# Optimization experiments

Measured on AMD Instinct MI355X. Metric: run time of the kernel, lower is better.

## Reference

```python
import jax, jax.numpy as jnp
import numpy as np

SIGMA = 5.0
KSIZE = 31  # int(6*sigma+1), odd
CHANNEL = 3

def build_gaussian_kernel(size, sigma):
    coords = jnp.arange(size, dtype=jnp.float32) - size // 2
    g = jnp.exp(-coords ** 2 / (2.0 * sigma ** 2))
    g = g / g.sum()
    k2d = g[:, None] * g[None, :]            # (k, k)
    # depthwise kernel: (O=C, I/g=1, k, k)
    return jnp.broadcast_to(k2d[None, None], (CHANNEL, 1, size, size))

def depthwise_blur(x, kernel):
    # x: (B, C, H, W); kernel: (C, 1, k, k); groups = C, SAME-style padding k//2
    pad = KSIZE // 2
    return jax.lax.conv_general_dilated(
        x, kernel,
        window_strides=(1, 1),
        padding=((pad, pad), (pad, pad)),
        dimension_numbers=("NCHW", "OIHW", "NCHW"),
        feature_group_count=CHANNEL,
    )

def setup_inputs() -> dict:
    key = jax.random.key(0)
    k1, k2 = jax.random.split(key)
    B, C, H, W = 16, 3, 512, 512
    background = jax.random.uniform(k1, (B, C, H, W), dtype=jnp.float32)
    insatance = jax.random.uniform(k2, (B, C, H, W), dtype=jnp.float32)
    gaussian_kernel = build_gaussian_kernel(KSIZE, SIGMA)
    return {"background": background, "insatance": insatance,
            "gaussian_kernel": gaussian_kernel}

def reference(background, insatance, gaussian_kernel):
    # retinex_decompose(background): only illumination1 is used downstream
    bg_log = jnp.log1p(background)
    illumination1 = depthwise_blur(bg_log, gaussian_kernel)
    # retinex_decompose(insatance): reflectance2 = log1p(ins) - blur(log1p(ins))
    ins_log = jnp.log1p(insatance)
    illumination2 = depthwise_blur(ins_log, gaussian_kernel)
    reflectance2 = ins_log - illumination2
    # adjust_illumination(reflectance2, illumination1)
    img_log = reflectance2 + illumination1
    img_corrected = jnp.clip(jnp.expm1(img_log), 0.0, 1.0)
    return img_corrected
```

## Files before the change

### kernel.cpp

```cpp
#include <hip/hip_runtime.h>


constexpr int W_    = 512;
constexpr int H_    = 512;
constexpr int NIMG  = 48;
constexpr int NROWS = NIMG * H_;

__device__ constexpr float G[31] = {
    8.8805851e-04f, 1.5861066e-03f, 2.7217699e-03f, 4.4874399e-03f,
    7.1084368e-03f, 1.0818767e-02f, 1.5820117e-02f, 2.2226435e-02f,
    3.0002549e-02f, 3.8911209e-02f, 4.8486352e-02f, 5.8048702e-02f,
    6.6771901e-02f, 7.3794364e-02f, 7.8357552e-02f, 7.9940480e-02f,
    7.8357552e-02f, 7.3794364e-02f, 6.6771901e-02f, 5.8048702e-02f,
    4.8486352e-02f, 3.8911209e-02f, 3.0002549e-02f, 2.2226435e-02f,
    1.5820117e-02f, 1.0818767e-02f, 7.1084368e-03f, 4.4874399e-03f,
    2.7217699e-03f, 1.5861066e-03f, 8.8805851e-04f};

__global__ __launch_bounds__(128) void hblur(const float* bg,
                                             const float* __restrict__ ins,
                                             float* tmp) {
  __shared__ __align__(16) float sh[544];
  const int tid = threadIdx.x;
  const size_t base = (size_t)blockIdx.x * W_;

  float4* s4w = (float4*)sh;
  if (tid < 8) {
    int s = (tid < 4) ? tid : (128 + tid);
    s4w[s] = make_float4(0.f, 0.f, 0.f, 0.f);
  }
  {
    float4 b = ((const float4*)(bg + base))[tid];
    float4 n = ((const float4*)(ins + base))[tid];
    float4 v;
    v.x = __logf(1.f + b.x) - __logf(1.f + n.x);
    v.y = __logf(1.f + b.y) - __logf(1.f + n.y);
    v.z = __logf(1.f + b.z) - __logf(1.f + n.z);
    v.w = __logf(1.f + b.w) - __logf(1.f + n.w);
    s4w[tid + 4] = v;
  }
  __syncthreads();

  float win[36];
  const float4* s4 = (const float4*)sh;
#pragma unroll
  for (int k = 0; k < 9; ++k) {
    float4 v = s4[tid + k];
    win[4 * k + 0] = v.x; win[4 * k + 1] = v.y;
    win[4 * k + 2] = v.z; win[4 * k + 3] = v.w;
  }
  float4 acc = make_float4(0.f, 0.f, 0.f, 0.f);
#pragma unroll
  for (int c = 0; c < 31; ++c) {
    acc.x += G[c] * win[1 + c];
    acc.y += G[c] * win[2 + c];
    acc.z += G[c] * win[3 + c];
    acc.w += G[c] * win[4 + c];
  }
  ((float4*)(tmp + base))[tid] = acc;
}

__global__ __launch_bounds__(256) void vblur(const float* __restrict__ tmp,
                                             const float* __restrict__ ins,
                                             float* __restrict__ out) {
  const int tx = threadIdx.x;
  const int x  = blockIdx.x * 64 + tx;
  const int y0 = blockIdx.y * 32 + threadIdx.y * 8;
  const size_t base = (size_t)blockIdx.z * ((size_t)H_ * W_);

  float acc[8] = {0.f, 0.f, 0.f, 0.f, 0.f, 0.f, 0.f, 0.f};
#pragma unroll
  for (int j = 0; j < 38; ++j) {
    const int yy = y0 - 15 + j;
    const float v = (yy >= 0 && yy < H_) ? tmp[base + (size_t)yy * W_ + x] : 0.f;
#pragma unroll
    for (int p = 0; p < 8; ++p) {
      const int c = j - p;
      if (c >= 0 && c < 31) acc[p] += G[c] * v;
    }
  }
#pragma unroll
  for (int p = 0; p < 8; ++p) {
    const size_t idx = base + (size_t)(y0 + p) * W_ + x;
    const float il = __logf(1.f + ins[idx]);
    float r = __expf(il + acc[p]) - 1.f;
    r = fminf(fmaxf(r, 0.f), 1.f);
    out[idx] = r;
  }
}

extern "C" void kernel_launch(void* const* d_in, const int* in_sizes, int n_in,
                              void* d_out, int out_size, void* d_ws, size_t ws_size,
                              hipStream_t stream) {
  const float* bg  = (const float*)d_in[0];
  const float* ins = (const float*)d_in[1];
  float* out = (float*)d_out;

  const size_t need = (size_t)NROWS * W_ * sizeof(float);
  float* tmp = (ws_size >= need) ? (float*)d_ws : (float*)d_in[0];

  hblur<<<dim3(NROWS), dim3(128), 0, stream>>>(bg, ins, tmp);
  vblur<<<dim3(8, 16, NIMG), dim3(64, 4, 1), 0, stream>>>(tmp, ins, out);
}
```

Measured before the change: 162.0 us.

## Fuse horizontal and vertical blur into one tiled kernel using shared memory

```diff
diff --git a/kernel.cpp b/kernel.cpp
--- a/kernel.cpp
+++ b/kernel.cpp
@@ -1,10 +1,13 @@
 #include <hip/hip_runtime.h>
 
 
-constexpr int W_    = 512;
-constexpr int H_    = 512;
-constexpr int NIMG  = 48;
-constexpr int NROWS = NIMG * H_;
+constexpr int W_ = 512, H_ = 512;
+constexpr int NIMG = 48;
+constexpr int TW = 64, TH = 64;
+constexpr int R_ = TH + 30;
+constexpr int CSLOT = 24;
+constexpr int DSTRIDE = 25;
+constexpr int HSTRIDE = 17;
 
 __device__ constexpr float G[31] = {
     8.8805851e-04f, 1.5861066e-03f, 2.7217699e-03f, 4.4874399e-03f,
@@ -16,75 +19,92 @@
     1.5820117e-02f, 1.0818767e-02f, 7.1084368e-03f, 4.4874399e-03f,
     2.7217699e-03f, 1.5861066e-03f, 8.8805851e-04f};
 
-__global__ __launch_bounds__(128) void hblur(const float* bg,
-                                             const float* __restrict__ ins,
-                                             float* tmp) {
-  __shared__ __align__(16) float sh[544];
+__global__ __launch_bounds__(256) void retinex_fused(const float* __restrict__ bg,
+                                                     const float* __restrict__ ins,
+                                                     float* __restrict__ out) {
+  __shared__ float4 sd[R_ * DSTRIDE];
+  __shared__ float4 sh[R_ * HSTRIDE];
+
   const int tid = threadIdx.x;
-  const size_t base = (size_t)blockIdx.x * W_;
+  const int x0 = blockIdx.x * TW;
+  const int y0 = blockIdx.y * TH;
+  const size_t base = (size_t)blockIdx.z * ((size_t)H_ * W_);
 
-  float4* s4w = (float4*)sh;
-  if (tid < 8) {
-    int s = (tid < 4) ? tid : (128 + tid);
-    s4w[s] = make_float4(0.f, 0.f, 0.f, 0.f);
-  }
-  {
-    float4 b = ((const float4*)(bg + base))[tid];
-    float4 n = ((const float4*)(ins + base))[tid];
-    float4 v;
-    v.x = __logf(1.f + b.x) - __logf(1.f + n.x);
-    v.y = __logf(1.f + b.y) - __logf(1.f + n.y);
-    v.z = __logf(1.f + b.z) - __logf(1.f + n.z);
-    v.w = __logf(1.f + b.w) - __logf(1.f + n.w);
-    s4w[tid + 4] = v;
+#pragma unroll
+  for (int it = 0; it < 9; ++it) {
+    const int idx = tid + 256 * it;
+    if (idx < R_ * CSLOT) {
+      const int r = idx / CSLOT;
+      const int c = idx - r * CSLOT;
+      const int y = y0 - 15 + r;
+      const int gx = x0 - 16 + 4 * c;
+      float4 v = make_float4(0.f, 0.f, 0.f, 0.f);
+      if ((unsigned)y < (unsigned)H_ && (unsigned)gx < (unsigned)W_) {
+        const size_t a = base + (size_t)y * W_ + gx;
+        const float4 b = *(const float4*)(bg + a);
+        const float4 n = *(const float4*)(ins + a);
+        v.x = __logf(1.f + b.x) - __logf(1.f + n.x);
+        v.y = __logf(1.f + b.y) - __logf(1.f + n.y);
+        v.z = __logf(1.f + b.z) - __logf(1.f + n.z);
+        v.w = __logf(1.f + b.w) - __logf(1.f + n.w);
+      }
+      sd[r * DSTRIDE + c] = v;
+    }
   }
   __syncthreads();
 
-  float win[36];
-  const float4* s4 = (const float4*)sh;
 #pragma unroll
-  for (int k = 0; k < 9; ++k) {
-    float4 v = s4[tid + k];
-    win[4 * k + 0] = v.x; win[4 * k + 1] = v.y;
-    win[4 * k + 2] = v.z; win[4 * k + 3] = v.w;
-  }
-  float4 acc = make_float4(0.f, 0.f, 0.f, 0.f);
+  for (int it = 0; it < 3; ++it) {
+    const int idx = tid + 256 * it;
+    if (idx < R_ * 8) {
+      const int r = idx >> 3;
+      const int w = idx & 7;
+      float win[40];
+      const float4* p = &sd[r * DSTRIDE + 2 * w];
 #pragma unroll
-  for (int c = 0; c < 31; ++c) {
-    acc.x += G[c] * win[1 + c];
-    acc.y += G[c] * win[2 + c];
-    acc.z += G[c] * win[3 + c];
-    acc.w += G[c] * win[4 + c];
-  }
-  ((float4*)(tmp + base))[tid] = acc;
-}
-
-__global__ __launch_bounds__(256) void vblur(const float* __restrict__ tmp,
-                                             const float* __restrict__ ins,
-                                             float* __restrict__ out) {
-  const int tx = threadIdx.x;
-  const int x  = blockIdx.x * 64 + tx;
-  const int y0 = blockIdx.y * 32 + threadIdx.y * 8;
-  const size_t base = (size_t)blockIdx.z * ((size_t)H_ * W_);
-
-  float acc[8] = {0.f, 0.f, 0.f, 0.f, 0.f, 0.f, 0.f, 0.f};
+      for (int k = 0; k < 10; ++k) {
+        const float4 v = p[k];
+        win[4 * k + 0] = v.x; win[4 * k + 1] = v.y;
+        win[4 * k + 2] = v.z; win[4 * k + 3] = v.w;
+      }
+      float o[8];
 #pragma unroll
-  for (int j = 0; j < 38; ++j) {
-    const int yy = y0 - 15 + j;
-    const float v = (yy >= 0 && yy < H_) ? tmp[base + (size_t)yy * W_ + x] : 0.f;
+      for (int e = 0; e < 8; ++e) {
+        float a = 0.f;
 #pragma unroll
-    for (int p = 0; p < 8; ++p) {
-      const int c = j - p;
-      if (c >= 0 && c < 31) acc[p] += G[c] * v;
+        for (int c = 0; c < 31; ++c) a += G[c] * win[e + 1 + c];
+        o[e] = a;
+      }
+      sh[r * HSTRIDE + 2 * w]     = make_float4(o[0], o[1], o[2], o[3]);
+      sh[r * HSTRIDE + 2 * w + 1] = make_float4(o[4], o[5], o[6], o[7]);
     }
   }
+  __syncthreads();
+
+  {
+    const int col = tid & 63;
+    const int g = tid >> 6;
+    const float* hf = (const float*)sh;
+    float acc[16];
 #pragma unroll
-  for (int p = 0; p < 8; ++p) {
-    const size_t idx = base + (size_t)(y0 + p) * W_ + x;
-    const float il = __logf(1.f + ins[idx]);
-    float r = __expf(il + acc[p]) - 1.f;
-    r = fminf(fmaxf(r, 0.f), 1.f);
-    out[idx] = r;
+    for (int p = 0; p < 16; ++p) acc[p] = 0.f;
+#pragma unroll
+    for (int j = 0; j < 46; ++j) {
+      const float v = hf[(16 * g + j) * (HSTRIDE * 4) + col];
+#pragma unroll
+      for (int p = 0; p < 16; ++p) {
+        const int c = j - p;
+        if (c >= 0 && c < 31) acc[p] += G[c] * v;
+      }
+    }
+#pragma unroll
+    for (int p = 0; p < 16; ++p) {
+      const int y = y0 + 16 * g + p;
+      const size_t idx = base + (size_t)y * W_ + x0 + col;
+      const float il = __logf(1.f + ins[idx]);
+      float r = __expf(il + acc[p]) - 1.f;
+      out[idx] = fminf(fmaxf(r, 0.f), 1.f);
+    }
   }
 }
 
@@ -94,10 +114,5 @@
   const float* bg  = (const float*)d_in[0];
   const float* ins = (const float*)d_in[1];
   float* out = (float*)d_out;
-
-  const size_t need = (size_t)NROWS * W_ * sizeof(float);
-  float* tmp = (ws_size >= need) ? (float*)d_ws : (float*)d_in[0];
-
-  hblur<<<dim3(NROWS), dim3(128), 0, stream>>>(bg, ins, tmp);
-  vblur<<<dim3(8, 16, NIMG), dim3(64, 4, 1), 0, stream>>>(tmp, ins, out);
+  retinex_fused<<<dim3(W_ / TW, H_ / TH, NIMG), dim3(256), 0, stream>>>(bg, ins, out);
 }
```

After: 188.8 us. 16.5% more time.
